# Optimization experiments

Hardware: AMD Instinct MI355X
Metric: run time of the kernel (lower is better)

Reference implementation:

```python
import jax, jax.numpy as jnp
import numpy as np

BLOCK_SIZE = 128  # tokens per row-block


def setup_inputs() -> dict:
    key = jax.random.key(0)
    k1, k2, k3, k4 = jax.random.split(key, 4)
    num_blocks = 64
    embed_dim, hidden_dim, output_dim = 4096, 16384, 4096
    num_nz = 32
    x = jax.random.normal(k1, (num_blocks * BLOCK_SIZE, embed_dim), dtype=jnp.float32)
    fc1_weight = jax.random.normal(k2, (embed_dim, hidden_dim), dtype=jnp.float32)
    fc2_weight = jax.random.normal(k3, (hidden_dim, output_dim), dtype=jnp.float32)
    # unique, sorted nonzero block indices
    nz = jnp.sort(jax.random.permutation(k4, num_blocks)[:num_nz]).astype(jnp.int32)
    return {
        "x": x,
        "fc1_weight": fc1_weight,
        "fc2_weight": fc2_weight,
        "NZ_BLOCK_INDICES": nz,
        "NUM_NZ_BLOCKS": num_nz,
    }


def reference(x, fc1_weight, fc2_weight, NZ_BLOCK_INDICES, NUM_NZ_BLOCKS):
    # Block-sparse MLP: only the row-blocks of x listed in NZ_BLOCK_INDICES are
    # computed; all other output blocks are zero (no bias, so zero blocks stay
    # zero through both layers).
    rows, embed_dim = x.shape
    num_blocks = rows // BLOCK_SIZE
    out_dim = fc2_weight.shape[1]
    nz = NZ_BLOCK_INDICES[:NUM_NZ_BLOCKS]  # [nnz]
    xb = x.reshape(num_blocks, BLOCK_SIZE, embed_dim)
    g = xb[nz]  # [nnz, B, D] gather only nonzero blocks
    h = jnp.einsum('nbd,dh->nbh', g, fc1_weight)   # fc1 on nonzero blocks only
    og = jnp.einsum('nbh,ho->nbo', h, fc2_weight)  # fc2 on nonzero blocks only
    out = jnp.zeros((num_blocks, BLOCK_SIZE, out_dim), dtype=x.dtype).at[nz].set(og)
    return out.reshape(rows, out_dim)
```

## Files before the change

kernel.cpp:

```cpp
#include <hip/hip_runtime.h>
#include <hip/hip_bf16.h>
#include <stdint.h>


typedef __attribute__((ext_vector_type(8))) _Float16 half8;
typedef __attribute__((ext_vector_type(4))) float f32x4;

__device__ __forceinline__ void gld_lds16(const void* g, void* l) {
    __builtin_amdgcn_global_load_lds(
        (const __attribute__((address_space(1))) unsigned int*)g,
        (__attribute__((address_space(3))) unsigned int*)l, 16, 0, 0);
}

__global__ __launch_bounds__(256) void zero_kernel(
    float* __restrict__ out, const int* __restrict__ nz, int nnz)
{
    const int OUTD = 4096;
    int b = blockIdx.x;
    bool active = false;
    for (int i = 0; i < nnz; ++i) active |= (nz[i] == b);
    if (active) return;
    float4* p = (float4*)(out + (size_t)b * 128 * OUTD);
    const int total = 128 * OUTD / 4;
    const float4 z = make_float4(0.f, 0.f, 0.f, 0.f);
    for (int i = threadIdx.x + blockIdx.y * 256; i < total; i += 256 * gridDim.y)
        p[i] = z;
}

__global__ __launch_bounds__(256) void convT_kernel(
    const float* __restrict__ src, _Float16* __restrict__ dst, int K, int N)
{
    __shared__ float t[64][65];
    const int nb = blockIdx.x * 64, kb = blockIdx.y * 64;
    const int tid = threadIdx.x;
    #pragma unroll
    for (int i = 0; i < 4; ++i) {
        int idx = tid + i * 256;
        int r = idx >> 4, c4 = (idx & 15) * 4;
        float4 v = *(const float4*)(src + (size_t)(kb + r) * N + nb + c4);
        t[r][c4 + 0] = v.x; t[r][c4 + 1] = v.y;
        t[r][c4 + 2] = v.z; t[r][c4 + 3] = v.w;
    }
    __syncthreads();
    #pragma unroll
    for (int i = 0; i < 2; ++i) {
        int idx = tid + i * 256;
        int rn = idx >> 3, c8 = (idx & 7) * 8;
        _Float16 tmp[8];
        #pragma unroll
        for (int j = 0; j < 8; ++j) tmp[j] = (_Float16)t[c8 + j][rn];
        *(uint4*)(dst + (size_t)(nb + rn) * K + kb + c8) = *(const uint4*)tmp;
    }
}

__global__ __launch_bounds__(256) void convx_kernel(
    const float* __restrict__ x, const int* __restrict__ nz, _Float16* __restrict__ xg)
{
    const int EMBED = 4096;
    int row = blockIdx.x;
    int blk = nz[row >> 7];
    const float* src = x + ((size_t)blk * 128 + (row & 127)) * EMBED;
    _Float16* dst = xg + (size_t)row * EMBED;
    for (int i = threadIdx.x; i < EMBED / 4; i += 256) {
        float4 v = *(const float4*)(src + i * 4);
        _Float16 tmp[4] = {(_Float16)v.x, (_Float16)v.y, (_Float16)v.z, (_Float16)v.w};
        *(uint2*)(dst + i * 4) = *(const uint2*)tmp;
    }
}

__global__ __launch_bounds__(256) void gemm1_f16_kernel(
    const _Float16* __restrict__ A,
    const _Float16* __restrict__ BT,
    _Float16* __restrict__ H)
{
    const int K = 4096, N = 16384;
    __shared__ __align__(16) _Float16 Asm[128 * 32];
    __shared__ __align__(16) _Float16 Bsm[128 * 32];
    const int tid = threadIdx.x;
    const int lane = tid & 63, wid = tid >> 6;
    const int m0 = blockIdx.x * 128, n0 = blockIdx.y * 128;

    const int c0 = tid, c1 = tid + 256;
    const _Float16* gA0 = A + (size_t)(m0 + (c0 >> 2)) * K + (c0 & 3) * 8;
    const _Float16* gA1 = A + (size_t)(m0 + (c1 >> 2)) * K + (c1 & 3) * 8;
    const _Float16* gB0 = BT + (size_t)(n0 + (c0 >> 2)) * K + (c0 & 3) * 8;
    const _Float16* gB1 = BT + (size_t)(n0 + (c1 >> 2)) * K + (c1 & 3) * 8;
    char* lA0 = (char*)Asm + c0 * 16; char* lA1 = (char*)Asm + c1 * 16;
    char* lB0 = (char*)Bsm + c0 * 16; char* lB1 = (char*)Bsm + c1 * 16;

    const int wm = (wid & 1) * 64, wn = (wid >> 1) * 64;
    const int fr = lane & 15, fq = lane >> 4;

    f32x4 acc[4][4];
    #pragma unroll
    for (int i = 0; i < 4; ++i)
        #pragma unroll
        for (int j = 0; j < 4; ++j) acc[i][j] = (f32x4)(0.f);

    for (int k0 = 0; k0 < K; k0 += 32) {
        gld_lds16(gA0 + k0, lA0); gld_lds16(gA1 + k0, lA1);
        gld_lds16(gB0 + k0, lB0); gld_lds16(gB1 + k0, lB1);
        __syncthreads();
        half8 af[4], bf[4];
        #pragma unroll
        for (int i = 0; i < 4; ++i)
            af[i] = *(const half8*)&Asm[(wm + i * 16 + fr) * 32 + fq * 8];
        #pragma unroll
        for (int j = 0; j < 4; ++j)
            bf[j] = *(const half8*)&Bsm[(wn + j * 16 + fr) * 32 + fq * 8];
        #pragma unroll
        for (int i = 0; i < 4; ++i)
            #pragma unroll
            for (int j = 0; j < 4; ++j)
                acc[i][j] = __builtin_amdgcn_mfma_f32_16x16x32_f16(af[i], bf[j], acc[i][j], 0, 0, 0);
        __syncthreads();
    }
    #pragma unroll
    for (int i = 0; i < 4; ++i)
        #pragma unroll
        for (int j = 0; j < 4; ++j)
            #pragma unroll
            for (int r = 0; r < 4; ++r) {
                int m = m0 + wm + i * 16 + fq * 4 + r;
                int n = n0 + wn + j * 16 + fr;
                H[(size_t)m * N + n] = (_Float16)acc[i][j][r];
            }
}

__global__ __launch_bounds__(256) void gemm2_f16_kernel(
    const _Float16* __restrict__ A,
    const _Float16* __restrict__ BT,
    const int* __restrict__ nz, float* __restrict__ out)
{
    const int K = 16384, N = 4096;
    __shared__ __align__(16) _Float16 Asm[128 * 32];
    __shared__ __align__(16) _Float16 Bsm[128 * 32];
    const int tid = threadIdx.x;
    const int lane = tid & 63, wid = tid >> 6;
    const int m0 = blockIdx.x * 128, n0 = blockIdx.y * 128;

    const int c0 = tid, c1 = tid + 256;
    const _Float16* gA0 = A + (size_t)(m0 + (c0 >> 2)) * K + (c0 & 3) * 8;
    const _Float16* gA1 = A + (size_t)(m0 + (c1 >> 2)) * K + (c1 & 3) * 8;
    const _Float16* gB0 = BT + (size_t)(n0 + (c0 >> 2)) * K + (c0 & 3) * 8;
    const _Float16* gB1 = BT + (size_t)(n0 + (c1 >> 2)) * K + (c1 & 3) * 8;
    char* lA0 = (char*)Asm + c0 * 16; char* lA1 = (char*)Asm + c1 * 16;
    char* lB0 = (char*)Bsm + c0 * 16; char* lB1 = (char*)Bsm + c1 * 16;

    const int wm = (wid & 1) * 64, wn = (wid >> 1) * 64;
    const int fr = lane & 15, fq = lane >> 4;

    f32x4 acc[4][4];
    #pragma unroll
    for (int i = 0; i < 4; ++i)
        #pragma unroll
        for (int j = 0; j < 4; ++j) acc[i][j] = (f32x4)(0.f);

    for (int k0 = 0; k0 < K; k0 += 32) {
        gld_lds16(gA0 + k0, lA0); gld_lds16(gA1 + k0, lA1);
        gld_lds16(gB0 + k0, lB0); gld_lds16(gB1 + k0, lB1);
        __syncthreads();
        half8 af[4], bf[4];
        #pragma unroll
        for (int i = 0; i < 4; ++i)
            af[i] = *(const half8*)&Asm[(wm + i * 16 + fr) * 32 + fq * 8];
        #pragma unroll
        for (int j = 0; j < 4; ++j)
            bf[j] = *(const half8*)&Bsm[(wn + j * 16 + fr) * 32 + fq * 8];
        #pragma unroll
        for (int i = 0; i < 4; ++i)
            #pragma unroll
            for (int j = 0; j < 4; ++j)
                acc[i][j] = __builtin_amdgcn_mfma_f32_16x16x32_f16(af[i], bf[j], acc[i][j], 0, 0, 0);
        __syncthreads();
    }
    const int nzb = nz[blockIdx.x];
    #pragma unroll
    for (int i = 0; i < 4; ++i)
        #pragma unroll
        for (int j = 0; j < 4; ++j)
            #pragma unroll
            for (int r = 0; r < 4; ++r) {
                int mloc = wm + i * 16 + fq * 4 + r;
                int n = n0 + wn + j * 16 + fr;
                out[((size_t)nzb * 128 + mloc) * N + n] = acc[i][j][r];
            }
}

#define TILE 128
#define BK16 16
#define LDSROW (TILE + 4)

__device__ inline unsigned short f2bf(float f) {
    unsigned int u = __float_as_uint(f);
    return (unsigned short)((u + 0x7FFFu + ((u >> 16) & 1u)) >> 16);
}

__global__ __launch_bounds__(256, 4) void gemm1_fp32_kernel(
    const float* __restrict__ x, const float* __restrict__ w1,
    const int* __restrict__ nz, unsigned short* __restrict__ h)
{
    const int EMBED = 4096, HIDDEN = 16384;
    __shared__ float As[BK16][LDSROW];
    __shared__ float Bs[BK16][LDSROW];
    const int by = blockIdx.x, bx = blockIdx.y;
    const int t = threadIdx.x, tx = t & 15, ty = t >> 4;
    const int blk = nz[by];
    const float* xsrc = x + (size_t)blk * 128 * EMBED;
    const int n0 = bx * TILE;
    float acc[8][8];
    #pragma unroll
    for (int i = 0; i < 8; ++i)
        #pragma unroll
        for (int j = 0; j < 8; ++j) acc[i][j] = 0.f;
    for (int k0 = 0; k0 < EMBED; k0 += BK16) {
        #pragma unroll
        for (int i = 0; i < 2; ++i) {
            int idx = t + i * 256, row = idx >> 2, kc = (idx & 3) << 2;
            const float4 v = *(const float4*)(xsrc + (size_t)row * EMBED + k0 + kc);
            As[kc][row] = v.x; As[kc + 1][row] = v.y; As[kc + 2][row] = v.z; As[kc + 3][row] = v.w;
        }
        #pragma unroll
        for (int i = 0; i < 2; ++i) {
            int idx = t + i * 256, kr = idx >> 5, nc = (idx & 31) << 2;
            *(float4*)&Bs[kr][nc] = *(const float4*)(w1 + (size_t)(k0 + kr) * HIDDEN + n0 + nc);
        }
        __syncthreads();
        #pragma unroll
        for (int kk = 0; kk < BK16; ++kk) {
            float a[8], b[8];
            *(float4*)&a[0] = *(const float4*)&As[kk][ty * 8];
            *(float4*)&a[4] = *(const float4*)&As[kk][ty * 8 + 4];
            *(float4*)&b[0] = *(const float4*)&Bs[kk][tx * 8];
            *(float4*)&b[4] = *(const float4*)&Bs[kk][tx * 8 + 4];
            #pragma unroll
            for (int i = 0; i < 8; ++i)
                #pragma unroll
                for (int j = 0; j < 8; ++j) acc[i][j] = fmaf(a[i], b[j], acc[i][j]);
        }
        __syncthreads();
    }
    #pragma unroll
    for (int i = 0; i < 8; ++i) {
        size_t row = (size_t)(by * TILE + ty * 8 + i);
        unsigned short tmp[8];
        #pragma unroll
        for (int j = 0; j < 8; ++j) tmp[j] = f2bf(acc[i][j]);
        *(uint4*)(h + row * HIDDEN + n0 + tx * 8) = *(const uint4*)tmp;
    }
}

__global__ __launch_bounds__(256, 4) void gemm2_fp32_kernel(
    const unsigned short* __restrict__ h, const float* __restrict__ w2,
    const int* __restrict__ nz, float* __restrict__ out)
{
    const int HIDDEN = 16384, OUTD = 4096;
    __shared__ float As[BK16][LDSROW];
    __shared__ float Bs[BK16][LDSROW];
    const int by = blockIdx.x, bx = blockIdx.y;
    const int t = threadIdx.x, tx = t & 15, ty = t >> 4;
    const unsigned short* hsrc = h + (size_t)by * TILE * HIDDEN;
    const int n0 = bx * TILE;
    float acc[8][8];
    #pragma unroll
    for (int i = 0; i < 8; ++i)
        #pragma unroll
        for (int j = 0; j < 8; ++j) acc[i][j] = 0.f;
    for (int k0 = 0; k0 < HIDDEN; k0 += BK16) {
        {
            int row = t >> 1, kc = (t & 1) << 3;
            uint4 v = *(const uint4*)(hsrc + (size_t)row * HIDDEN + k0 + kc);
            unsigned int w[4] = {v.x, v.y, v.z, v.w};
            #pragma unroll
            for (int q = 0; q < 4; ++q) {
                As[kc + 2 * q][row] = __uint_as_float(w[q] << 16);
                As[kc + 2 * q + 1][row] = __uint_as_float(w[q] & 0xFFFF0000u);
            }
        }
        #pragma unroll
        for (int i = 0; i < 2; ++i) {
            int idx = t + i * 256, kr = idx >> 5, nc = (idx & 31) << 2;
            *(float4*)&Bs[kr][nc] = *(const float4*)(w2 + (size_t)(k0 + kr) * OUTD + n0 + nc);
        }
        __syncthreads();
        #pragma unroll
        for (int kk = 0; kk < BK16; ++kk) {
            float a[8], b[8];
            *(float4*)&a[0] = *(const float4*)&As[kk][ty * 8];
            *(float4*)&a[4] = *(const float4*)&As[kk][ty * 8 + 4];
            *(float4*)&b[0] = *(const float4*)&Bs[kk][tx * 8];
            *(float4*)&b[4] = *(const float4*)&Bs[kk][tx * 8 + 4];
            #pragma unroll
            for (int i = 0; i < 8; ++i)
                #pragma unroll
                for (int j = 0; j < 8; ++j) acc[i][j] = fmaf(a[i], b[j], acc[i][j]);
        }
        __syncthreads();
    }
    const int blk = nz[by];
    #pragma unroll
    for (int i = 0; i < 8; ++i) {
        size_t orow = (size_t)blk * TILE + ty * 8 + i;
        float* dst = out + orow * OUTD + n0 + tx * 8;
        *(float4*)dst = make_float4(acc[i][0], acc[i][1], acc[i][2], acc[i][3]);
        *(float4*)(dst + 4) = make_float4(acc[i][4], acc[i][5], acc[i][6], acc[i][7]);
    }
}

extern "C" void kernel_launch(void* const* d_in, const int* in_sizes, int n_in,
                              void* d_out, int out_size, void* d_ws, size_t ws_size,
                              hipStream_t stream) {
    const float* x  = (const float*)d_in[0];
    const float* w1 = (const float*)d_in[1];
    const float* w2 = (const float*)d_in[2];
    const int* nz   = (const int*)d_in[3];
    const int nnz   = in_sizes[3];
    float* out = (float*)d_out;

    const int EMBED = 4096, HIDDEN = 16384, OUTD = 4096;
    const int rows = in_sizes[0] / EMBED;
    const int nblocks = rows / 128;
    const int arows = nnz * 128;

    const size_t MiB = 1024 * 1024;
    const size_t offXG = 0;
    const size_t offW1T = 32 * MiB;
    const size_t offW2T = 160 * MiB;
    const size_t offH = 288 * MiB;
    const size_t need = 416 * MiB;

    zero_kernel<<<dim3(nblocks, 32), 256, 0, stream>>>(out, nz, nnz);

    if (ws_size >= need) {
        _Float16* xg  = (_Float16*)((char*)d_ws + offXG);
        _Float16* w1t = (_Float16*)((char*)d_ws + offW1T);
        _Float16* w2t = (_Float16*)((char*)d_ws + offW2T);
        _Float16* h   = (_Float16*)((char*)d_ws + offH);
        convT_kernel<<<dim3(HIDDEN / 64, EMBED / 64), 256, 0, stream>>>(w1, w1t, EMBED, HIDDEN);
        convT_kernel<<<dim3(OUTD / 64, HIDDEN / 64), 256, 0, stream>>>(w2, w2t, HIDDEN, OUTD);
        convx_kernel<<<dim3(arows), 256, 0, stream>>>(x, nz, xg);
        gemm1_f16_kernel<<<dim3(arows / 128, HIDDEN / 128), 256, 0, stream>>>(xg, w1t, h);
        gemm2_f16_kernel<<<dim3(arows / 128, OUTD / 128), 256, 0, stream>>>(h, w2t, nz, out);
    } else {
        unsigned short* h = (unsigned short*)d_ws;
        gemm1_fp32_kernel<<<dim3(nnz, HIDDEN / TILE), 256, 0, stream>>>(x, w1, nz, h);
        gemm2_fp32_kernel<<<dim3(nnz, OUTD / TILE), 256, 0, stream>>>(h, w2, nz, out);
    }
}
```

Measured before the change: 2.160 ms.

## Replace f16 GEMMs with 256x256 tiled, multi-buffered, swizzled MFMA kernel

Result: faster. 2.007 ms (-7.1%).

```diff
diff --git a/kernel.cpp b/kernel.cpp
--- a/kernel.cpp
+++ b/kernel.cpp
@@ -68,123 +68,144 @@
     }
 }
 
-__global__ __launch_bounds__(256) void gemm1_f16_kernel(
+template<int K, int N, bool SCATTER>
+__global__ __launch_bounds__(512, 2) void gemm256_kernel(
     const _Float16* __restrict__ A,
     const _Float16* __restrict__ BT,
-    _Float16* __restrict__ H)
-{
-    const int K = 4096, N = 16384;
-    __shared__ __align__(16) _Float16 Asm[128 * 32];
-    __shared__ __align__(16) _Float16 Bsm[128 * 32];
+    const int* __restrict__ nz,
+    void* __restrict__ outp)
+{
+    const int MTILES = 16;
+    const int NTILES = N / 256;
+    const int nwg = MTILES * NTILES;
+    int bid = blockIdx.x;
+    int swz = (bid & 7) * (nwg >> 3) + (bid >> 3);
+    const int m0 = (swz % MTILES) * 256;
+    const int n0 = (swz / MTILES) * 256;
+
+    __shared__ __align__(16) _Float16 As[4][256 * 32];
+    __shared__ __align__(16) _Float16 Bs[4][256 * 32];
+
     const int tid = threadIdx.x;
-    const int lane = tid & 63, wid = tid >> 6;
-    const int m0 = blockIdx.x * 128, n0 = blockIdx.y * 128;
-
-    const int c0 = tid, c1 = tid + 256;
-    const _Float16* gA0 = A + (size_t)(m0 + (c0 >> 2)) * K + (c0 & 3) * 8;
-    const _Float16* gA1 = A + (size_t)(m0 + (c1 >> 2)) * K + (c1 & 3) * 8;
-    const _Float16* gB0 = BT + (size_t)(n0 + (c0 >> 2)) * K + (c0 & 3) * 8;
-    const _Float16* gB1 = BT + (size_t)(n0 + (c1 >> 2)) * K + (c1 & 3) * 8;
-    char* lA0 = (char*)Asm + c0 * 16; char* lA1 = (char*)Asm + c1 * 16;
-    char* lB0 = (char*)Bsm + c0 * 16; char* lB1 = (char*)Bsm + c1 * 16;
-
-    const int wm = (wid & 1) * 64, wn = (wid >> 1) * 64;
+    const int lane = tid & 63;
+    const int wid = tid >> 6;
+    const int wr = wid >> 2;
+    const int wc = wid & 3;
     const int fr = lane & 15, fq = lane >> 4;
-
-    f32x4 acc[4][4];
-    #pragma unroll
-    for (int i = 0; i < 4; ++i)
+    const int slotsw = fq ^ ((fr >> 1) & 3);
+
+    const int s0 = tid, s1 = tid + 512;
+    const int ar0 = s0 >> 2, al0 = (s0 & 3) ^ ((ar0 >> 1) & 3);
+    const int ar1 = s1 >> 2, al1 = (s1 & 3) ^ ((ar1 >> 1) & 3);
+    const _Float16* gA0 = A + (size_t)(m0 + ar0) * K + al0 * 8;
+    const _Float16* gA1 = A + (size_t)(m0 + ar1) * K + al1 * 8;
+    const _Float16* gB0 = BT + (size_t)(n0 + ar0) * K + al0 * 8;
+    const _Float16* gB1 = BT + (size_t)(n0 + ar1) * K + al1 * 8;
+
+    const int aOff = (wr * 128 + fr) * 32 + slotsw * 8;
+    const int bOff = (wc * 64 + fr) * 32 + slotsw * 8;
+
+    f32x4 acc[8][4];
+    #pragma unroll
+    for (int i = 0; i < 8; ++i)
         #pragma unroll
         for (int j = 0; j < 4; ++j) acc[i][j] = (f32x4)(0.f);
 
-    for (int k0 = 0; k0 < K; k0 += 32) {
-        gld_lds16(gA0 + k0, lA0); gld_lds16(gA1 + k0, lA1);
-        gld_lds16(gB0 + k0, lB0); gld_lds16(gB1 + k0, lB1);
-        __syncthreads();
-        half8 af[4], bf[4];
+    const int NKT = K / 32;
+
+    #pragma unroll
+    for (int t = 0; t < 2; ++t) {
+        char* la = (char*)&As[t][0];
+        char* lb = (char*)&Bs[t][0];
+        gld_lds16(gA0 + t * 32, la + s0 * 16);
+        gld_lds16(gA1 + t * 32, la + s1 * 16);
+        gld_lds16(gB0 + t * 32, lb + s0 * 16);
+        gld_lds16(gB1 + t * 32, lb + s1 * 16);
+    }
+    asm volatile("s_waitcnt vmcnt(4)" ::: "memory");
+    __builtin_amdgcn_s_barrier();
+
+    for (int t = 0; t < NKT; ++t) {
+        const _Float16* as = &As[t & 3][0];
+        const _Float16* bs = &Bs[t & 3][0];
+        half8 afr[4], bfr[4];
+
         #pragma unroll
         for (int i = 0; i < 4; ++i)
-            af[i] = *(const half8*)&Asm[(wm + i * 16 + fr) * 32 + fq * 8];
+            afr[i] = *(const half8*)(as + aOff + i * 512);
         #pragma unroll
         for (int j = 0; j < 4; ++j)
-            bf[j] = *(const half8*)&Bsm[(wn + j * 16 + fr) * 32 + fq * 8];
+            bfr[j] = *(const half8*)(bs + bOff + j * 512);
+        if (t + 2 < NKT) {
+            char* la = (char*)&As[(t + 2) & 3][0];
+            gld_lds16(gA0 + (t + 2) * 32, la + s0 * 16);
+            gld_lds16(gA1 + (t + 2) * 32, la + s1 * 16);
+        }
+        __builtin_amdgcn_s_barrier();
+        asm volatile("s_waitcnt lgkmcnt(0)" ::: "memory");
+        __builtin_amdgcn_sched_barrier(0);
+        __builtin_amdgcn_s_setprio(1);
         #pragma unroll
         for (int i = 0; i < 4; ++i)
             #pragma unroll
             for (int j = 0; j < 4; ++j)
-                acc[i][j] = __builtin_amdgcn_mfma_f32_16x16x32_f16(af[i], bf[j], acc[i][j], 0, 0, 0);
-        __syncthreads();
-    }
-    #pragma unroll
-    for (int i = 0; i < 4; ++i)
-        #pragma unroll
-        for (int j = 0; j < 4; ++j)
-            #pragma unroll
-            for (int r = 0; r < 4; ++r) {
-                int m = m0 + wm + i * 16 + fq * 4 + r;
-                int n = n0 + wn + j * 16 + fr;
-                H[(size_t)m * N + n] = (_Float16)acc[i][j][r];
+                acc[i][j] = __builtin_amdgcn_mfma_f32_16x16x32_f16(afr[i], bfr[j], acc[i][j], 0, 0, 0);
+        __builtin_amdgcn_s_setprio(0);
+        __builtin_amdgcn_s_barrier();
+
+        #pragma unroll
+        for (int i = 0; i < 4; ++i)
+            afr[i] = *(const half8*)(as + aOff + 2048 + i * 512);
+        if (t + 2 < NKT) {
+            char* lb = (char*)&Bs[(t + 2) & 3][0];
+            gld_lds16(gB0 + (t + 2) * 32, lb + s0 * 16);
+            gld_lds16(gB1 + (t + 2) * 32, lb + s1 * 16);
+        }
+        __builtin_amdgcn_s_barrier();
+        asm volatile("s_waitcnt lgkmcnt(0)" ::: "memory");
+        __builtin_amdgcn_sched_barrier(0);
+        __builtin_amdgcn_s_setprio(1);
+        #pragma unroll
+        for (int i = 0; i < 4; ++i)
+            #pragma unroll
+            for (int j = 0; j < 4; ++j)
+                acc[4 + i][j] = __builtin_amdgcn_mfma_f32_16x16x32_f16(afr[i], bfr[j], acc[4 + i][j], 0, 0, 0);
+        __builtin_amdgcn_s_setprio(0);
+        if (t == NKT - 2) { asm volatile("s_waitcnt vmcnt(0)" ::: "memory"); }
+        else              { asm volatile("s_waitcnt vmcnt(4)" ::: "memory"); }
+        __builtin_amdgcn_s_barrier();
+    }
+
+    if (!SCATTER) {
+        _Float16* H = (_Float16*)outp;
+        #pragma unroll
+        for (int idx = 0; idx < 8; ++idx) {
+            int mbase = m0 + wr * 128 + (idx >> 2) * 64 + (idx & 3) * 16 + fq * 4;
+            #pragma unroll
+            for (int j = 0; j < 4; ++j) {
+                int n = n0 + wc * 64 + j * 16 + fr;
+                #pragma unroll
+                for (int r = 0; r < 4; ++r)
+                    H[(size_t)(mbase + r) * N + n] = (_Float16)acc[idx][j][r];
             }
-}
-
-__global__ __launch_bounds__(256) void gemm2_f16_kernel(
-    const _Float16* __restrict__ A,
-    const _Float16* __restrict__ BT,
-    const int* __restrict__ nz, float* __restrict__ out)
-{
-    const int K = 16384, N = 4096;
-    __shared__ __align__(16) _Float16 Asm[128 * 32];
-    __shared__ __align__(16) _Float16 Bsm[128 * 32];
-    const int tid = threadIdx.x;
-    const int lane = tid & 63, wid = tid >> 6;
-    const int m0 = blockIdx.x * 128, n0 = blockIdx.y * 128;
-
-    const int c0 = tid, c1 = tid + 256;
-    const _Float16* gA0 = A + (size_t)(m0 + (c0 >> 2)) * K + (c0 & 3) * 8;
-    const _Float16* gA1 = A + (size_t)(m0 + (c1 >> 2)) * K + (c1 & 3) * 8;
-    const _Float16* gB0 = BT + (size_t)(n0 + (c0 >> 2)) * K + (c0 & 3) * 8;
-    const _Float16* gB1 = BT + (size_t)(n0 + (c1 >> 2)) * K + (c1 & 3) * 8;
-    char* lA0 = (char*)Asm + c0 * 16; char* lA1 = (char*)Asm + c1 * 16;
-    char* lB0 = (char*)Bsm + c0 * 16; char* lB1 = (char*)Bsm + c1 * 16;
-
-    const int wm = (wid & 1) * 64, wn = (wid >> 1) * 64;
-    const int fr = lane & 15, fq = lane >> 4;
-
-    f32x4 acc[4][4];
-    #pragma unroll
-    for (int i = 0; i < 4; ++i)
-        #pragma unroll
-        for (int j = 0; j < 4; ++j) acc[i][j] = (f32x4)(0.f);
-
-    for (int k0 = 0; k0 < K; k0 += 32) {
-        gld_lds16(gA0 + k0, lA0); gld_lds16(gA1 + k0, lA1);
-        gld_lds16(gB0 + k0, lB0); gld_lds16(gB1 + k0, lB1);
-        __syncthreads();
-        half8 af[4], bf[4];
-        #pragma unroll
-        for (int i = 0; i < 4; ++i)
-            af[i] = *(const half8*)&Asm[(wm + i * 16 + fr) * 32 + fq * 8];
-        #pragma unroll
-        for (int j = 0; j < 4; ++j)
-            bf[j] = *(const half8*)&Bsm[(wn + j * 16 + fr) * 32 + fq * 8];
-        #pragma unroll
-        for (int i = 0; i < 4; ++i)
-            #pragma unroll
-            for (int j = 0; j < 4; ++j)
-                acc[i][j] = __builtin_amdgcn_mfma_f32_16x16x32_f16(af[i], bf[j], acc[i][j], 0, 0, 0);
-        __syncthreads();
-    }
-    const int nzb = nz[blockIdx.x];
-    #pragma unroll
-    for (int i = 0; i < 4; ++i)
-        #pragma unroll
-        for (int j = 0; j < 4; ++j)
-            #pragma unroll
-            for (int r = 0; r < 4; ++r) {
-                int mloc = wm + i * 16 + fq * 4 + r;
-                int n = n0 + wn + j * 16 + fr;
-                out[((size_t)nzb * 128 + mloc) * N + n] = acc[i][j][r];
+        }
+    } else {
+        float* out = (float*)outp;
+        const int nzA = nz[m0 >> 7];
+        const int nzB = nz[(m0 >> 7) + 1];
+        const int blk = wr ? nzB : nzA;
+        #pragma unroll
+        for (int idx = 0; idx < 8; ++idx) {
+            int lm = (idx >> 2) * 64 + (idx & 3) * 16 + fq * 4;
+            #pragma unroll
+            for (int j = 0; j < 4; ++j) {
+                int n = n0 + wc * 64 + j * 16 + fr;
+                #pragma unroll
+                for (int r = 0; r < 4; ++r)
+                    out[((size_t)blk * 128 + lm + r) * N + n] = acc[idx][j][r];
             }
+        }
+    }
 }
 
 #define TILE 128
@@ -331,7 +352,7 @@
 
     zero_kernel<<<dim3(nblocks, 32), 256, 0, stream>>>(out, nz, nnz);
 
-    if (ws_size >= need) {
+    if (ws_size >= need && arows == 4096) {
         _Float16* xg  = (_Float16*)((char*)d_ws + offXG);
         _Float16* w1t = (_Float16*)((char*)d_ws + offW1T);
         _Float16* w2t = (_Float16*)((char*)d_ws + offW2T);
@@ -339,8 +360,8 @@
         convT_kernel<<<dim3(HIDDEN / 64, EMBED / 64), 256, 0, stream>>>(w1, w1t, EMBED, HIDDEN);
         convT_kernel<<<dim3(OUTD / 64, HIDDEN / 64), 256, 0, stream>>>(w2, w2t, HIDDEN, OUTD);
         convx_kernel<<<dim3(arows), 256, 0, stream>>>(x, nz, xg);
-        gemm1_f16_kernel<<<dim3(arows / 128, HIDDEN / 128), 256, 0, stream>>>(xg, w1t, h);
-        gemm2_f16_kernel<<<dim3(arows / 128, OUTD / 128), 256, 0, stream>>>(h, w2t, nz, out);
+        gemm256_kernel<4096, 16384, false><<<dim3(16 * (16384 / 256)), 512, 0, stream>>>(xg, w1t, nullptr, h);
+        gemm256_kernel<16384, 4096, true><<<dim3(16 * (4096 / 256)), 512, 0, stream>>>(h, w2t, nz, out);
     } else {
         unsigned short* h = (unsigned short*)d_ws;
         gemm1_fp32_kernel<<<dim3(nnz, HIDDEN / TILE), 256, 0, stream>>>(x, w1, nz, h);
```
